# Kernel tuning notes

Hardware: AMD Instinct MI355X
Metric: run time of the kernel (lower is better)

## Reference

```python
import jax, jax.numpy as jnp
import numpy as np

C = 64
C2 = C // 2

def setup_inputs() -> dict:
    key = jax.random.key(0)
    ks = jax.random.split(key, 5)
    x = jax.random.normal(ks[0], (8, C, 64, 64), dtype=jnp.float32)
    # 1x1 conv weights stored as [out, in] matrices (kernel size 1)
    g_w = jax.random.normal(ks[1], (C2, C), dtype=jnp.float32) * (1.0 / np.sqrt(C))
    g_b = jax.random.normal(ks[2], (C2,), dtype=jnp.float32) * 0.01
    W_w = jax.random.normal(ks[3], (C, C2), dtype=jnp.float32) * (1.0 / np.sqrt(C2))
    W_b = jax.random.normal(ks[4], (C,), dtype=jnp.float32) * 0.01
    return {"x": x, "g_w": g_w, "g_b": g_b, "W_w": W_w, "W_b": W_b}

def reference(x, g_w, g_b, W_w, W_b):
    b, c, h, w = x.shape
    xf = x.reshape(b, c, h * w)                      # [B, C, N]
    # g: 1x1 conv -> [B, N, C2]
    g_x = jnp.einsum('oc,bcn->bno', g_w, xf) + g_b
    # attention scores on raw x (theta/phi convs unused in original forward)
    f = jnp.einsum('bcn,bcm->bnm', xf, xf)           # [B, N, N]
    f_div_C = jax.nn.softmax(f, axis=-1)
    y = jnp.einsum('bnm,bmo->bno', f_div_C, g_x)     # [B, N, C2]
    # W: 1x1 conv back to C channels, then residual
    W_y = jnp.einsum('co,bno->bcn', W_w, y) + W_b[None, :, None]
    z = W_y.reshape(b, c, h, w) + x
    return z
```

## Files before the change

### kernel.cpp

```cpp
#include <hip/hip_runtime.h>
#include <hip/hip_bf16.h>

#define BATCH 8
#define CH    64
#define CH2   32
#define NN    4096
#define BN    (BATCH * NN)
#define KPAD  72
#define VPAD  136
#define YPAD  36
#define RPAD  40
#define MAXSPLIT 8

typedef __attribute__((ext_vector_type(8)))  short        short8;
typedef __attribute__((ext_vector_type(4)))  float        floatx4;
typedef __attribute__((ext_vector_type(16))) float        floatx16;
typedef __attribute__((ext_vector_type(4)))  unsigned int uint4v;
typedef __attribute__((ext_vector_type(8)))  unsigned short ushort8v;
typedef __attribute__((ext_vector_type(4)))  unsigned short ushort4v;
typedef unsigned short ushort_t;

#define LOG2E      1.4426950408889634f
#define SQRT_LOG2E 1.2011224087864498f

__device__ __forceinline__ unsigned short f2bf_rne(float f) {
    unsigned int u = __float_as_uint(f);
    return (unsigned short)((u + 0x7FFFu + ((u >> 16) & 1u)) >> 16);
}

__global__ __launch_bounds__(256) void prep_fused(const float* __restrict__ x,
                                                  const float* __restrict__ gw,
                                                  const float* __restrict__ gb,
                                                  ushort_t* __restrict__ xT,
                                                  float* __restrict__ mlog,
                                                  ushort_t* __restrict__ gxT) {
    __shared__ float gwl[CH2 * CH];
    __shared__ float gbl[CH2];
    __shared__ float xl[CH][33];

    const int t = threadIdx.x;
    for (int i = t; i < CH2 * CH; i += 256) gwl[i] = gw[i];
    if (t < CH2) gbl[t] = gb[t];

    const int b  = blockIdx.x >> 7;
    const int n0 = (blockIdx.x & 127) * 32;

    {
        const int nl = t & 31, cg = (t >> 5) * 8;
        const float* xpp = x + ((size_t)b * CH + cg) * NN + n0 + nl;
        #pragma unroll
        for (int j = 0; j < 8; ++j) xl[cg + j][nl] = xpp[(size_t)j * NN];
    }
    __syncthreads();

    const int row = t >> 3;
    const int o8  = t & 7;
    const int n   = n0 + row;
    const int growg = b * NN + n;

    float xv[8];
    #pragma unroll
    for (int j = 0; j < 8; ++j) xv[j] = xl[o8 * 8 + j][row];

    float ns = 0.f;
    short8 v0;
    #pragma unroll
    for (int j = 0; j < 8; ++j) {
        ns += xv[j] * xv[j];
        v0[j] = (short)f2bf_rne(xv[j] * SQRT_LOG2E);
    }
    *(short8*)(xT + (size_t)growg * CH + o8 * 8) = v0;
    ns += __shfl_xor(ns, 1);
    ns += __shfl_xor(ns, 2);
    ns += __shfl_xor(ns, 4);
    if (o8 == 0) mlog[growg] = 12.0f * sqrtf(ns) * LOG2E;

    float acc[CH2];
    #pragma unroll
    for (int o = 0; o < CH2; ++o) {
        const float4* wr = (const float4*)(gwl + o * CH + o8 * 8);
        float4 w0 = wr[0], w1 = wr[1];
        acc[o] = w0.x * xv[0] + w0.y * xv[1] + w0.z * xv[2] + w0.w * xv[3]
               + w1.x * xv[4] + w1.y * xv[5] + w1.z * xv[6] + w1.w * xv[7];
    }
    #pragma unroll
    for (int o = 0; o < CH2; ++o) {
        acc[o] += __shfl_xor(acc[o], 1);
        acc[o] += __shfl_xor(acc[o], 2);
        acc[o] += __shfl_xor(acc[o], 4);
    }
    #pragma unroll
    for (int i = 0; i < 4; ++i) {
        int o = o8 * 4 + i;
        gxT[((size_t)b * CH2 + o) * NN + n] = f2bf_rne(acc[o] + gbl[o]);
    }
}

__global__ __launch_bounds__(256, 4) void flash_attn(const ushort_t* __restrict__ xT,
                                                     const ushort_t* __restrict__ gxT,
                                                     const float* __restrict__ mlog,
                                                     ushort_t* __restrict__ py,
                                                     float* __restrict__ pl,
                                                     int ksplit) {
    __shared__ __align__(16) unsigned char smem[(128 * KPAD + 32 * VPAD) * 2];
    ushort_t* Klds = (ushort_t*)smem;
    ushort_t* Vlds = Klds + 128 * KPAD;

    const int tid = threadIdx.x, wave = tid >> 6, lane = tid & 63;
    const int q5 = lane & 31;
    const int h  = lane >> 5;
    const int bq = blockIdx.x & 255;
    const int sp = blockIdx.x >> 8;
    const int b = bq >> 5, qt = bq & 31;
    const int n0 = qt * 128 + wave * 32;
    const int k0 = sp * ksplit;

    short8 qf[4];
    {
        const ushort_t* qp = xT + ((size_t)(b * NN + n0 + q5)) * CH + h * 8;
        #pragma unroll
        for (int f = 0; f < 4; ++f) qf[f] = *(const short8*)(qp + f * 16);
    }
    const float ml = mlog[(size_t)b * NN + n0 + q5];

    floatx16 mlC;
    #pragma unroll
    for (int i = 0; i < 16; ++i) mlC[i] = -ml;

    floatx16 yt;
    #pragma unroll
    for (int i = 0; i < 16; ++i) yt[i] = 0.f;
    float lsum = 0.f;

    const ushort_t* kb = xT + (size_t)(b * NN + k0) * CH;
    const ushort_t* vb = gxT + (size_t)b * CH2 * NN + k0;
    const int iters = ksplit >> 7;
    const int skey = tid >> 3, sc0 = (tid & 7) * 8;
    const int vc0 = (tid & 7) * 16;

    for (int kt = 0; kt < iters; ++kt) {
        const size_t kof = (size_t)kt << 13;
        short8 gk0 = *(const short8*)(kb + kof + (size_t)(skey     ) * CH + sc0);
        short8 gk1 = *(const short8*)(kb + kof + (size_t)(skey + 32) * CH + sc0);
        short8 gk2 = *(const short8*)(kb + kof + (size_t)(skey + 64) * CH + sc0);
        short8 gk3 = *(const short8*)(kb + kof + (size_t)(skey + 96) * CH + sc0);
        short8 gv0 = *(const short8*)(vb + (size_t)skey * NN + kt * 128 + vc0);
        short8 gv1 = *(const short8*)(vb + (size_t)skey * NN + kt * 128 + vc0 + 8);

        __syncthreads();
        *(short8*)(&Klds[(skey     ) * KPAD + sc0]) = gk0;
        *(short8*)(&Klds[(skey + 32) * KPAD + sc0]) = gk1;
        *(short8*)(&Klds[(skey + 64) * KPAD + sc0]) = gk2;
        *(short8*)(&Klds[(skey + 96) * KPAD + sc0]) = gk3;
        *(short8*)(&Vlds[skey * VPAD + vc0])     = gv0;
        *(short8*)(&Vlds[skey * VPAD + vc0 + 8]) = gv1;
        __syncthreads();

        #pragma unroll
        for (int T = 0; T < 4; ++T) {
            floatx16 st;
            __builtin_amdgcn_s_setprio(1);
            {
                short8 kf = *(const short8*)(&Klds[(T * 32 + q5) * KPAD + h * 8]);
                st = __builtin_amdgcn_mfma_f32_32x32x16_bf16(kf, qf[0], mlC, 0, 0, 0);
            }
            #pragma unroll
            for (int f = 1; f < 4; ++f) {
                short8 kf = *(const short8*)(&Klds[(T * 32 + q5) * KPAD + f * 16 + h * 8]);
                st = __builtin_amdgcn_mfma_f32_32x32x16_bf16(kf, qf[f], st, 0, 0, 0);
            }
            __builtin_amdgcn_s_setprio(0);
            unsigned int d[8];
            #pragma unroll
            for (int r2 = 0; r2 < 8; ++r2) {
                float p0 = __builtin_amdgcn_exp2f(st[2 * r2]);
                float p1 = __builtin_amdgcn_exp2f(st[2 * r2 + 1]);
                lsum += p0;
                lsum += p1;
                unsigned int pk;
                asm("v_cvt_pk_bf16_f32 %0, %1, %2" : "=v"(pk) : "v"(p0), "v"(p1));
                d[r2] = pk;
            }
            #pragma unroll
            for (int fp = 0; fp < 2; ++fp) {
                unsigned int b0 = d[fp * 4 + 0], b1 = d[fp * 4 + 1];
                unsigned int b2 = d[fp * 4 + 2], b3 = d[fp * 4 + 3];
                asm("v_permlane32_swap_b32 %0, %1" : "+v"(b0), "+v"(b2));
                asm("v_permlane32_swap_b32 %0, %1" : "+v"(b1), "+v"(b3));
                uint4v bv;
                bv[0] = b0; bv[1] = b1; bv[2] = b2; bv[3] = b3;
                short8 pb = __builtin_bit_cast(short8, bv);
                short8 vf = *(const short8*)(&Vlds[q5 * VPAD + T * 32 + fp * 16 + h * 8]);
                __builtin_amdgcn_s_setprio(1);
                yt = __builtin_amdgcn_mfma_f32_32x32x16_bf16(vf, pb, yt, 0, 0, 0);
                __builtin_amdgcn_s_setprio(0);
            }
        }
    }

    lsum += __shfl_xor(lsum, 32);

    __syncthreads();
    float* yb = (float*)smem + wave * 32 * YPAD;
    #pragma unroll
    for (int reg = 0; reg < 16; ++reg) {
        int o = (reg & 3) + 8 * (reg >> 2) + 4 * h;
        yb[q5 * YPAD + o] = yt[reg];
    }
    __syncthreads();
    {
        int qq = lane >> 1, half = lane & 1;
        const float* src = yb + qq * YPAD + half * 16;
        float4 s0 = *(const float4*)(src);
        float4 s1 = *(const float4*)(src + 4);
        float4 s2 = *(const float4*)(src + 8);
        float4 s3 = *(const float4*)(src + 12);
        ushort8v pk0, pk1;
        pk0[0] = f2bf_rne(s0.x); pk0[1] = f2bf_rne(s0.y);
        pk0[2] = f2bf_rne(s0.z); pk0[3] = f2bf_rne(s0.w);
        pk0[4] = f2bf_rne(s1.x); pk0[5] = f2bf_rne(s1.y);
        pk0[6] = f2bf_rne(s1.z); pk0[7] = f2bf_rne(s1.w);
        pk1[0] = f2bf_rne(s2.x); pk1[1] = f2bf_rne(s2.y);
        pk1[2] = f2bf_rne(s2.z); pk1[3] = f2bf_rne(s2.w);
        pk1[4] = f2bf_rne(s3.x); pk1[5] = f2bf_rne(s3.y);
        pk1[6] = f2bf_rne(s3.z); pk1[7] = f2bf_rne(s3.w);
        ushort_t* dst = py + ((size_t)sp * BN + (size_t)b * NN + n0 + qq) * CH2 + half * 16;
        *(ushort8v*)(dst)     = pk0;
        *(ushort8v*)(dst + 8) = pk1;
    }
    if (h == 0) pl[(size_t)sp * BN + (size_t)b * NN + n0 + q5] = lsum;
}

__global__ __launch_bounds__(512) void reduce_proj(const ushort_t* __restrict__ py,
                                                   const float* __restrict__ pl,
                                                   const float* __restrict__ Ww,
                                                   const float* __restrict__ Wb,
                                                   const float* __restrict__ x,
                                                   float* __restrict__ out,
                                                   int nsplit) {
    __shared__ ushort_t WwB[CH * RPAD];
    __shared__ ushort_t Y[64 * RPAD];
    __shared__ float    linv[64];
    __shared__ float    WbL[CH];

    const int t = threadIdx.x;
    const int grow0 = blockIdx.x * 64;

    if (t < 256) {
        const int r = t >> 2, o8 = (t & 3) * 8;
        const float* wp = Ww + r * CH2 + o8;
        ushort8v w;
        #pragma unroll
        for (int j = 0; j < 8; ++j) w[j] = f2bf_rne(wp[j]);
        *(ushort8v*)(&WwB[r * RPAD + o8]) = w;
    }
    if (t < CH) WbL[t] = Wb[t];
    if (t < 64) {
        const float* plp = pl + grow0 + t;
        float lv[MAXSPLIT];
        #pragma unroll
        for (int s = 0; s < MAXSPLIT; ++s) {
            int sc = s < nsplit ? s : 0;
            lv[s] = plp[(size_t)sc * BN];
        }
        float l = 0.f;
        #pragma unroll
        for (int s = 0; s < MAXSPLIT; ++s) if (s < nsplit) l += lv[s];
        linv[t] = 1.0f / l;
    }

    const int row = t >> 3, o4 = (t & 7) * 4;
    float acc[4] = {0.f, 0.f, 0.f, 0.f};
    {
        const ushort_t* pp = py + (size_t)(grow0 + row) * CH2 + o4;
        ushort4v pv[MAXSPLIT];
        #pragma unroll
        for (int s = 0; s < MAXSPLIT; ++s) {
            int sc = s < nsplit ? s : 0;
            pv[s] = *(const ushort4v*)(pp + (size_t)sc * BN * CH2);
        }
        #pragma unroll
        for (int s = 0; s < MAXSPLIT; ++s) if (s < nsplit) {
            #pragma unroll
            for (int j = 0; j < 4; ++j)
                acc[j] += __uint_as_float((unsigned int)pv[s][j] << 16);
        }
    }
    __syncthreads();
    {
        float inv = linv[row];
        ushort4v yv;
        #pragma unroll
        for (int j = 0; j < 4; ++j) yv[j] = f2bf_rne(acc[j] * inv);
        *(ushort4v*)(&Y[row * RPAD + o4]) = yv;
    }
    __syncthreads();

    const int wave = t >> 6, lane = t & 63;
    const int ql = lane & 15, quad = lane >> 4;
    const int nt = wave & 3;
    const int ctb = (wave >> 2) * 2;
    const int b = grow0 >> 12;
    const int nbase = (grow0 & (NN - 1)) + nt * 16;

    short8 bfrag = *(const short8*)(&Y[(nt * 16 + ql) * RPAD + quad * 8]);
    #pragma unroll
    for (int ci = 0; ci < 2; ++ci) {
        int ct = ctb + ci;
        short8 afrag = *(const short8*)(&WwB[(ct * 16 + ql) * RPAD + quad * 8]);
        floatx4 d = (floatx4){0.f, 0.f, 0.f, 0.f};
        d = __builtin_amdgcn_mfma_f32_16x16x32_bf16(afrag, bfrag, d, 0, 0, 0);
        #pragma unroll
        for (int r = 0; r < 4; ++r) {
            int c = ct * 16 + quad * 4 + r;
            size_t oi = ((size_t)b * CH + c) * NN + nbase + ql;
            out[oi] = d[r] + WbL[c] + x[oi];
        }
    }
}

extern "C" void kernel_launch(void* const* d_in, const int* in_sizes, int n_in,
                              void* d_out, int out_size, void* d_ws, size_t ws_size,
                              hipStream_t stream) {
    const float* x  = (const float*)d_in[0];
    const float* gw = (const float*)d_in[1];
    const float* gb = (const float*)d_in[2];
    const float* Ww = (const float*)d_in[3];
    const float* Wb = (const float*)d_in[4];
    float* out = (float*)d_out;

    ushort_t* xT   = (ushort_t*)d_ws;
    ushort_t* gxT  = xT + (size_t)BN * CH;
    float*    mlog = (float*)(gxT + (size_t)BATCH * CH2 * NN);
    ushort_t* py   = (ushort_t*)(mlog + BN);
    size_t base_bytes = (size_t)BN * CH * 2 + (size_t)BATCH * CH2 * NN * 2 + (size_t)BN * 4;
    int split = MAXSPLIT;
    while (split > 1 && base_bytes + (size_t)split * BN * (CH2 * 2 + 4) > ws_size)
        split >>= 1;
    float* pl = (float*)(py + (size_t)split * BN * CH2);

    hipLaunchKernelGGL(prep_fused,  dim3(BN / 32),     dim3(256), 0, stream,
                       x, gw, gb, xT, mlog, gxT);
    hipLaunchKernelGGL(flash_attn,  dim3(256 * split), dim3(256), 0, stream,
                       xT, gxT, mlog, py, pl, NN / split);
    hipLaunchKernelGGL(reduce_proj, dim3(BN / 64),     dim3(512), 0, stream,
                       py, pl, Ww, Wb, x, out, split);
}
```

Before: 117.6 us.

## Store K/V in MFMA fragment-native layout and load directly from global, dropping LDS staging

The prep kernel now writes the bf16 keys and the g-projection values in a pre-swizzled layout that matches the MFMA operand fragments. Each wave of the attention kernel can then load its K and V fragments straight from global memory, with no LDS staging and no per-tile __syncthreads. This is meant to remove barrier stalls and LDS traffic, at the cost of every wave reading K/V on its own with no sharing across the block, which leans on L2/L1 for reuse. The reduce kernel also moves to 256 threads, each handling 8 channels with wider loads and 4 MFMAs per wave.

```diff
diff --git a/kernel.cpp b/kernel.cpp
--- a/kernel.cpp
+++ b/kernel.cpp
@@ -6,8 +6,6 @@
 #define CH2   32
 #define NN    4096
 #define BN    (BATCH * NN)
-#define KPAD  72
-#define VPAD  136
 #define YPAD  36
 #define RPAD  40
 #define MAXSPLIT 8
@@ -17,7 +15,6 @@
 typedef __attribute__((ext_vector_type(16))) float        floatx16;
 typedef __attribute__((ext_vector_type(4)))  unsigned int uint4v;
 typedef __attribute__((ext_vector_type(8)))  unsigned short ushort8v;
-typedef __attribute__((ext_vector_type(4)))  unsigned short ushort4v;
 typedef unsigned short ushort_t;
 
 #define LOG2E      1.4426950408889634f
@@ -28,12 +25,13 @@
     return (unsigned short)((u + 0x7FFFu + ((u >> 16) & 1u)) >> 16);
 }
 
+
 __global__ __launch_bounds__(256) void prep_fused(const float* __restrict__ x,
                                                   const float* __restrict__ gw,
                                                   const float* __restrict__ gb,
-                                                  ushort_t* __restrict__ xT,
+                                                  ushort_t* __restrict__ xF,
                                                   float* __restrict__ mlog,
-                                                  ushort_t* __restrict__ gxT) {
+                                                  ushort_t* __restrict__ gxF) {
     __shared__ float gwl[CH2 * CH];
     __shared__ float gbl[CH2];
     __shared__ float xl[CH][33];
@@ -69,7 +67,10 @@
         ns += xv[j] * xv[j];
         v0[j] = (short)f2bf_rne(xv[j] * SQRT_LOG2E);
     }
-    *(short8*)(xT + (size_t)growg * CH + o8 * 8) = v0;
+    {
+        size_t plane = (((size_t)b * 128 + (n0 >> 5)) * 4 + (o8 >> 1)) * 2 + (o8 & 1);
+        *(short8*)(xF + plane * 256 + row * 8) = v0;
+    }
     ns += __shfl_xor(ns, 1);
     ns += __shfl_xor(ns, 2);
     ns += __shfl_xor(ns, 4);
@@ -89,22 +90,23 @@
         acc[o] += __shfl_xor(acc[o], 2);
         acc[o] += __shfl_xor(acc[o], 4);
     }
-    #pragma unroll
-    for (int i = 0; i < 4; ++i) {
-        int o = o8 * 4 + i;
-        gxT[((size_t)b * CH2 + o) * NN + n] = f2bf_rne(acc[o] + gbl[o]);
-    }
-}
-
-__global__ __launch_bounds__(256, 4) void flash_attn(const ushort_t* __restrict__ xT,
-                                                     const ushort_t* __restrict__ gxT,
+    {
+        size_t vbase = (((size_t)b * 256 + (n >> 4)) * 2 + ((n >> 3) & 1)) * 256 + (n & 7);
+        #pragma unroll
+        for (int i = 0; i < 4; ++i) {
+            int o = o8 * 4 + i;
+            gxF[vbase + o * 8] = f2bf_rne(acc[o] + gbl[o]);
+        }
+    }
+}
+
+__global__ __launch_bounds__(256, 4) void flash_attn(const ushort_t* __restrict__ xF,
+                                                     const ushort_t* __restrict__ gxF,
                                                      const float* __restrict__ mlog,
                                                      ushort_t* __restrict__ py,
                                                      float* __restrict__ pl,
                                                      int ksplit) {
-    __shared__ __align__(16) unsigned char smem[(128 * KPAD + 32 * VPAD) * 2];
-    ushort_t* Klds = (ushort_t*)smem;
-    ushort_t* Vlds = Klds + 128 * KPAD;
+    __shared__ __align__(16) unsigned char smem[18432];
 
     const int tid = threadIdx.x, wave = tid >> 6, lane = tid & 63;
     const int q5 = lane & 31;
@@ -117,9 +119,9 @@
 
     short8 qf[4];
     {
-        const ushort_t* qp = xT + ((size_t)(b * NN + n0 + q5)) * CH + h * 8;
-        #pragma unroll
-        for (int f = 0; f < 4; ++f) qf[f] = *(const short8*)(qp + f * 16);
+        const ushort_t* qp = xF + ((((size_t)b * 128 + qt * 4 + wave) * 4) * 2 + h) * 256 + q5 * 8;
+        #pragma unroll
+        for (int f = 0; f < 4; ++f) qf[f] = *(const short8*)(qp + f * 512);
     }
     const float ml = mlog[(size_t)b * NN + n0 + q5];
 
@@ -132,75 +134,56 @@
     for (int i = 0; i < 16; ++i) yt[i] = 0.f;
     float lsum = 0.f;
 
-    const ushort_t* kb = xT + (size_t)(b * NN + k0) * CH;
-    const ushort_t* vb = gxT + (size_t)b * CH2 * NN + k0;
-    const int iters = ksplit >> 7;
-    const int skey = tid >> 3, sc0 = (tid & 7) * 8;
-    const int vc0 = (tid & 7) * 16;
-
-    for (int kt = 0; kt < iters; ++kt) {
-        const size_t kof = (size_t)kt << 13;
-        short8 gk0 = *(const short8*)(kb + kof + (size_t)(skey     ) * CH + sc0);
-        short8 gk1 = *(const short8*)(kb + kof + (size_t)(skey + 32) * CH + sc0);
-        short8 gk2 = *(const short8*)(kb + kof + (size_t)(skey + 64) * CH + sc0);
-        short8 gk3 = *(const short8*)(kb + kof + (size_t)(skey + 96) * CH + sc0);
-        short8 gv0 = *(const short8*)(vb + (size_t)skey * NN + kt * 128 + vc0);
-        short8 gv1 = *(const short8*)(vb + (size_t)skey * NN + kt * 128 + vc0 + 8);
-
-        __syncthreads();
-        *(short8*)(&Klds[(skey     ) * KPAD + sc0]) = gk0;
-        *(short8*)(&Klds[(skey + 32) * KPAD + sc0]) = gk1;
-        *(short8*)(&Klds[(skey + 64) * KPAD + sc0]) = gk2;
-        *(short8*)(&Klds[(skey + 96) * KPAD + sc0]) = gk3;
-        *(short8*)(&Vlds[skey * VPAD + vc0])     = gv0;
-        *(short8*)(&Vlds[skey * VPAD + vc0 + 8]) = gv1;
-        __syncthreads();
-
-        #pragma unroll
-        for (int T = 0; T < 4; ++T) {
-            floatx16 st;
+    const int nsub = ksplit >> 5;
+    const int r32base = k0 >> 5;
+    const int n16base = k0 >> 4;
+    const ushort_t* kp = xF + ((((size_t)b * 128 + r32base) * 4) * 2 + h) * 256 + q5 * 8;
+    const ushort_t* vp = gxF + (((size_t)b * 256 + n16base) * 2 + h) * 256 + q5 * 8;
+
+    #pragma unroll 2
+    for (int s = 0; s < nsub; ++s) {
+        const ushort_t* kps = kp + (size_t)s * 2048;
+        floatx16 st;
+        __builtin_amdgcn_s_setprio(1);
+        {
+            short8 kf = *(const short8*)(kps);
+            st = __builtin_amdgcn_mfma_f32_32x32x16_bf16(kf, qf[0], mlC, 0, 0, 0);
+        }
+        #pragma unroll
+        for (int f = 1; f < 4; ++f) {
+            short8 kf = *(const short8*)(kps + f * 512);
+            st = __builtin_amdgcn_mfma_f32_32x32x16_bf16(kf, qf[f], st, 0, 0, 0);
+        }
+        __builtin_amdgcn_s_setprio(0);
+        unsigned int d[8];
+        #pragma unroll
+        for (int r2 = 0; r2 < 8; ++r2) {
+            float p0 = __builtin_amdgcn_exp2f(st[2 * r2]);
+            float p1 = __builtin_amdgcn_exp2f(st[2 * r2 + 1]);
+            lsum += p0;
+            lsum += p1;
+            unsigned int pk;
+            asm("v_cvt_pk_bf16_f32 %0, %1, %2" : "=v"(pk) : "v"(p0), "v"(p1));
+            d[r2] = pk;
+        }
+        #pragma unroll
+        for (int fp = 0; fp < 2; ++fp) {
+            unsigned int b0 = d[fp * 4 + 0], b1 = d[fp * 4 + 1];
+            unsigned int b2 = d[fp * 4 + 2], b3 = d[fp * 4 + 3];
+            asm("v_permlane32_swap_b32 %0, %1" : "+v"(b0), "+v"(b2));
+            asm("v_permlane32_swap_b32 %0, %1" : "+v"(b1), "+v"(b3));
+            uint4v bv;
+            bv[0] = b0; bv[1] = b1; bv[2] = b2; bv[3] = b3;
+            short8 pb = __builtin_bit_cast(short8, bv);
+            short8 vf = *(const short8*)(vp + (size_t)(s * 2 + fp) * 512);
             __builtin_amdgcn_s_setprio(1);
-            {
-                short8 kf = *(const short8*)(&Klds[(T * 32 + q5) * KPAD + h * 8]);
-                st = __builtin_amdgcn_mfma_f32_32x32x16_bf16(kf, qf[0], mlC, 0, 0, 0);
-            }
-            #pragma unroll
-            for (int f = 1; f < 4; ++f) {
-                short8 kf = *(const short8*)(&Klds[(T * 32 + q5) * KPAD + f * 16 + h * 8]);
-                st = __builtin_amdgcn_mfma_f32_32x32x16_bf16(kf, qf[f], st, 0, 0, 0);
-            }
+            yt = __builtin_amdgcn_mfma_f32_32x32x16_bf16(vf, pb, yt, 0, 0, 0);
             __builtin_amdgcn_s_setprio(0);
-            unsigned int d[8];
-            #pragma unroll
-            for (int r2 = 0; r2 < 8; ++r2) {
-                float p0 = __builtin_amdgcn_exp2f(st[2 * r2]);
-                float p1 = __builtin_amdgcn_exp2f(st[2 * r2 + 1]);
-                lsum += p0;
-                lsum += p1;
-                unsigned int pk;
-                asm("v_cvt_pk_bf16_f32 %0, %1, %2" : "=v"(pk) : "v"(p0), "v"(p1));
-                d[r2] = pk;
-            }
-            #pragma unroll
-            for (int fp = 0; fp < 2; ++fp) {
-                unsigned int b0 = d[fp * 4 + 0], b1 = d[fp * 4 + 1];
-                unsigned int b2 = d[fp * 4 + 2], b3 = d[fp * 4 + 3];
-                asm("v_permlane32_swap_b32 %0, %1" : "+v"(b0), "+v"(b2));
-                asm("v_permlane32_swap_b32 %0, %1" : "+v"(b1), "+v"(b3));
-                uint4v bv;
-                bv[0] = b0; bv[1] = b1; bv[2] = b2; bv[3] = b3;
-                short8 pb = __builtin_bit_cast(short8, bv);
-                short8 vf = *(const short8*)(&Vlds[q5 * VPAD + T * 32 + fp * 16 + h * 8]);
-                __builtin_amdgcn_s_setprio(1);
-                yt = __builtin_amdgcn_mfma_f32_32x32x16_bf16(vf, pb, yt, 0, 0, 0);
-                __builtin_amdgcn_s_setprio(0);
-            }
         }
     }
 
     lsum += __shfl_xor(lsum, 32);
 
-    __syncthreads();
     float* yb = (float*)smem + wave * 32 * YPAD;
     #pragma unroll
     for (int reg = 0; reg < 16; ++reg) {
@@ -231,7 +214,7 @@
     if (h == 0) pl[(size_t)sp * BN + (size_t)b * NN + n0 + q5] = lsum;
 }
 
-__global__ __launch_bounds__(512) void reduce_proj(const ushort_t* __restrict__ py,
+__global__ __launch_bounds__(256) void reduce_proj(const ushort_t* __restrict__ py,
                                                    const float* __restrict__ pl,
                                                    const float* __restrict__ Ww,
                                                    const float* __restrict__ Wb,
@@ -244,15 +227,15 @@
     __shared__ float    WbL[CH];
 
     const int t = threadIdx.x;
+    const int row = t >> 2, o8 = (t & 3) * 8;
     const int grow0 = blockIdx.x * 64;
 
-    if (t < 256) {
-        const int r = t >> 2, o8 = (t & 3) * 8;
-        const float* wp = Ww + r * CH2 + o8;
+    {
+        const float* wp = Ww + row * CH2 + o8;
         ushort8v w;
         #pragma unroll
         for (int j = 0; j < 8; ++j) w[j] = f2bf_rne(wp[j]);
-        *(ushort8v*)(&WwB[r * RPAD + o8]) = w;
+        *(ushort8v*)(&WwB[row * RPAD + o8]) = w;
     }
     if (t < CH) WbL[t] = Wb[t];
     if (t < 64) {
@@ -269,44 +252,42 @@
         linv[t] = 1.0f / l;
     }
 
-    const int row = t >> 3, o4 = (t & 7) * 4;
-    float acc[4] = {0.f, 0.f, 0.f, 0.f};
-    {
-        const ushort_t* pp = py + (size_t)(grow0 + row) * CH2 + o4;
-        ushort4v pv[MAXSPLIT];
+    float acc[8];
+    #pragma unroll
+    for (int j = 0; j < 8; ++j) acc[j] = 0.f;
+    {
+        const ushort_t* pp = py + ((size_t)(grow0 + row)) * CH2 + o8;
+        ushort8v pv[MAXSPLIT];
         #pragma unroll
         for (int s = 0; s < MAXSPLIT; ++s) {
             int sc = s < nsplit ? s : 0;
-            pv[s] = *(const ushort4v*)(pp + (size_t)sc * BN * CH2);
+            pv[s] = *(const ushort8v*)(pp + (size_t)sc * BN * CH2);
         }
         #pragma unroll
         for (int s = 0; s < MAXSPLIT; ++s) if (s < nsplit) {
             #pragma unroll
-            for (int j = 0; j < 4; ++j)
+            for (int j = 0; j < 8; ++j)
                 acc[j] += __uint_as_float((unsigned int)pv[s][j] << 16);
         }
     }
     __syncthreads();
     {
         float inv = linv[row];
-        ushort4v yv;
-        #pragma unroll
-        for (int j = 0; j < 4; ++j) yv[j] = f2bf_rne(acc[j] * inv);
-        *(ushort4v*)(&Y[row * RPAD + o4]) = yv;
+        ushort8v yv;
+        #pragma unroll
+        for (int j = 0; j < 8; ++j) yv[j] = f2bf_rne(acc[j] * inv);
+        *(ushort8v*)(&Y[row * RPAD + o8]) = yv;
     }
     __syncthreads();
 
     const int wave = t >> 6, lane = t & 63;
     const int ql = lane & 15, quad = lane >> 4;
-    const int nt = wave & 3;
-    const int ctb = (wave >> 2) * 2;
     const int b = grow0 >> 12;
-    const int nbase = (grow0 & (NN - 1)) + nt * 16;
-
-    short8 bfrag = *(const short8*)(&Y[(nt * 16 + ql) * RPAD + quad * 8]);
-    #pragma unroll
-    for (int ci = 0; ci < 2; ++ci) {
-        int ct = ctb + ci;
+    const int nbase = (grow0 & (NN - 1)) + wave * 16;
+
+    short8 bfrag = *(const short8*)(&Y[(wave * 16 + ql) * RPAD + quad * 8]);
+    #pragma unroll
+    for (int ct = 0; ct < 4; ++ct) {
         short8 afrag = *(const short8*)(&WwB[(ct * 16 + ql) * RPAD + quad * 8]);
         floatx4 d = (floatx4){0.f, 0.f, 0.f, 0.f};
         d = __builtin_amdgcn_mfma_f32_16x16x32_bf16(afrag, bfrag, d, 0, 0, 0);
@@ -329,9 +310,9 @@
     const float* Wb = (const float*)d_in[4];
     float* out = (float*)d_out;
 
-    ushort_t* xT   = (ushort_t*)d_ws;
-    ushort_t* gxT  = xT + (size_t)BN * CH;
-    float*    mlog = (float*)(gxT + (size_t)BATCH * CH2 * NN);
+    ushort_t* xF   = (ushort_t*)d_ws;
+    ushort_t* gxF  = xF + (size_t)BN * CH;
+    float*    mlog = (float*)(gxF + (size_t)BATCH * CH2 * NN);
     ushort_t* py   = (ushort_t*)(mlog + BN);
     size_t base_bytes = (size_t)BN * CH * 2 + (size_t)BATCH * CH2 * NN * 2 + (size_t)BN * 4;
     int split = MAXSPLIT;
@@ -340,9 +321,9 @@
     float* pl = (float*)(py + (size_t)split * BN * CH2);
 
     hipLaunchKernelGGL(prep_fused,  dim3(BN / 32),     dim3(256), 0, stream,
-                       x, gw, gb, xT, mlog, gxT);
+                       x, gw, gb, xF, mlog, gxF);
     hipLaunchKernelGGL(flash_attn,  dim3(256 * split), dim3(256), 0, stream,
-                       xT, gxT, mlog, py, pl, NN / split);
-    hipLaunchKernelGGL(reduce_proj, dim3(BN / 64),     dim3(512), 0, stream,
+                       xF, gxF, mlog, py, pl, NN / split);
+    hipLaunchKernelGGL(reduce_proj, dim3(BN / 64),     dim3(256), 0, stream,
                        py, pl, Ww, Wb, x, out, split);
 }
```

After: 124.0 us. 1.05x slower.
